# Performance work log

Measured on AMD Instinct MI355X. Metric: run time of the kernel, lower is better.

Reference implementation:

```python
import jax, jax.numpy as jnp
import numpy as np

# --- CSV_Architecture_v2 layout (mediapipe hands: 21 landmarks per hand) ---
INTRO = np.arange(0, 3)                 # vector_intro_idxs
H0_IDX, H0_PROB = 3, 4                  # handedness_0_idx, handedness_0_prob_idx
HAND0_X = np.arange(5, 26)
HAND0_Y = np.arange(26, 47)
HAND0_Z = np.arange(47, 68)
H1_IDX, H1_PROB = 68, 69
HAND1_X = np.arange(70, 91)
HAND1_Y = np.arange(91, 112)
HAND1_Z = np.arange(112, 133)
FRAME_REPR_LEN = 133
NO_HAND = -1.0                          # arch.no_hand_detected_val

B, S = 256, 2048


def setup_inputs() -> dict:
    key = jax.random.key(0)
    k1, k2, k3 = jax.random.split(key, 3)
    X = jax.random.normal(k1, (B, S, FRAME_REPR_LEN), dtype=jnp.float32)
    h0 = jnp.where(jax.random.bernoulli(k2, 0.3, (B, S)), NO_HAND, 1.0)
    h1 = jnp.where(jax.random.bernoulli(k3, 0.3, (B, S)), NO_HAND, 1.0)
    X = X.at[:, :, H0_IDX].set(h0).at[:, :, H1_IDX].set(h1)
    return {"X": X}


def _hand_sub_matrix(x, hidx, xi, yi, zi):
    """x: [S, F]. Build the per-hand subtraction matrix of strategy 'seq_on_last':
    find the MOST RECENT frame where this hand is valid, take its wrist (x,y,z),
    and subtract that wrist from this hand's coord columns on every valid frame."""
    S = x.shape[0]
    valid = x[:, hidx] != NO_HAND                      # [S] bool
    any_valid = jnp.any(valid)
    t = jnp.arange(S)
    last = jnp.maximum(jnp.max(jnp.where(valid, t, -1)), 0)  # last valid frame (safe)
    wrist_cols = jnp.array([xi[0], yi[0], zi[0]])
    ref = x[last, wrist_cols]                          # [3] reference wrist
    sub_vec = (jnp.zeros((x.shape[1],), x.dtype)
               .at[xi].set(ref[0])
               .at[yi].set(ref[1])
               .at[zi].set(ref[2]))                    # [F]
    row_mask = (valid & any_valid).astype(x.dtype)     # subtract only on valid frames
    return row_mask[:, None] * sub_vec[None, :]        # [S, F]


def reference(X):
    """Strategy 'seq_on_last': per sequence, per hand, normalize coords to the
    most recent valid wrist point. Vectorized over batch (original: tf.map_fn)."""
    def per_seq(x):  # x: [S, F]
        s0 = _hand_sub_matrix(x, H0_IDX, HAND0_X, HAND0_Y, HAND0_Z)
        s1 = _hand_sub_matrix(x, H1_IDX, HAND1_X, HAND1_Y, HAND1_Z)
        return x - (s0 + s1)
    return jax.vmap(per_seq)(X)
```

## Files before the change

kernel.cpp:

```cpp
#include <hip/hip_runtime.h>

#define SEQ 2048
#define FR  133
#define H0I 3
#define H1I 68
#define NOHAND -1.0f
#define BLK 1024

__global__ __launch_bounds__(BLK) void normalizer_kernel(
    const float* __restrict__ X, float* __restrict__ Out) {
    __shared__ unsigned char s_mask[SEQ];
    __shared__ float s_ref[6];
    __shared__ int s_red0[16], s_red1[16];

    const int b   = blockIdx.x;
    const int tid = threadIdx.x;
    const float* xb = X   + (size_t)b * (SEQ * FR);
    float*       ob = Out + (size_t)b * (SEQ * FR);

    int m0 = -1, m1 = -1;
    for (int t = tid; t < SEQ; t += BLK) {
        float v0 = xb[(size_t)t * FR + H0I];
        float v1 = xb[(size_t)t * FR + H1I];
        int b0 = (v0 != NOHAND);
        int b1 = (v1 != NOHAND);
        s_mask[t] = (unsigned char)(b0 | (b1 << 1));
        if (b0) m0 = t;
        if (b1) m1 = t;
    }
    #pragma unroll
    for (int off = 32; off > 0; off >>= 1) {
        m0 = max(m0, __shfl_down(m0, off, 64));
        m1 = max(m1, __shfl_down(m1, off, 64));
    }
    int wave = tid >> 6, lane = tid & 63;
    if (lane == 0) { s_red0[wave] = m0; s_red1[wave] = m1; }
    __syncthreads();
    if (tid == 0) {
        int a0 = -1, a1 = -1;
        #pragma unroll
        for (int w = 0; w < BLK / 64; ++w) {
            a0 = max(a0, s_red0[w]);
            a1 = max(a1, s_red1[w]);
        }
        int l0 = a0 < 0 ? 0 : a0;
        int l1 = a1 < 0 ? 0 : a1;
        s_ref[0] = xb[(size_t)l0 * FR + 5];
        s_ref[1] = xb[(size_t)l0 * FR + 26];
        s_ref[2] = xb[(size_t)l0 * FR + 47];
        s_ref[3] = xb[(size_t)l1 * FR + 70];
        s_ref[4] = xb[(size_t)l1 * FR + 91];
        s_ref[5] = xb[(size_t)l1 * FR + 112];
    }
    __syncthreads();
    const float r0x = s_ref[0], r0y = s_ref[1], r0z = s_ref[2];
    const float r1x = s_ref[3], r1y = s_ref[4], r1z = s_ref[5];

    const int NV = (SEQ * FR) / 4;
    const float4* xv = (const float4*)xb;
    float4*       ov = (float4*)ob;
    for (int i = tid; i < NV; i += BLK) {
        float4 v = xv[i];
        int e     = i * 4;
        int frame = (int)((unsigned)e / 133u);
        int f0    = e - frame * 133;
        float vals[4] = {v.x, v.y, v.z, v.w};
        #pragma unroll
        for (int j = 0; j < 4; ++j) {
            int f = f0 + j;
            int fr = frame;
            if (f >= FR) { f -= FR; fr += 1; }
            int mk = s_mask[fr];
            float sub = 0.f;
            if (f >= 5 && f < 68) {
                if (mk & 1) {
                    int k = (f >= 26) + (f >= 47);
                    sub = (k == 0) ? r0x : ((k == 1) ? r0y : r0z);
                }
            } else if (f >= 70) {
                if (mk & 2) {
                    int k = (f >= 91) + (f >= 112);
                    sub = (k == 0) ? r1x : ((k == 1) ? r1y : r1z);
                }
            }
            vals[j] -= sub;
        }
        float4 o; o.x = vals[0]; o.y = vals[1]; o.z = vals[2]; o.w = vals[3];
        ov[i] = o;
    }
}

extern "C" void kernel_launch(void* const* d_in, const int* in_sizes, int n_in,
                              void* d_out, int out_size, void* d_ws, size_t ws_size,
                              hipStream_t stream) {
    const float* X = (const float*)d_in[0];
    float* Out     = (float*)d_out;
    int nB = in_sizes[0] / (SEQ * FR);
    normalizer_kernel<<<nB, BLK, 0, stream>>>(X, Out);
}
```

Measured before the change: 125.0 us.

## Split into backward-scan refs kernel and chunked streaming kernel

Replaces the single per-sequence block with two kernels. The first uses one wave per sequence that scans backward with ballots and stops at the most recent valid frame for each hand, then writes the six wrist references to workspace. The second launches eight blocks per sequence, each handling a 256-frame chunk with its own local mask, which raises parallelism beyond the 256 blocks of the old launch. This adds a second launch and a workspace round trip, and the backward scan reads strided handedness values.

After: 127.6 us. 2.1% more time.

```diff
diff --git a/kernel.cpp b/kernel.cpp
--- a/kernel.cpp
+++ b/kernel.cpp
@@ -5,61 +5,70 @@
 #define H0I 3
 #define H1I 68
 #define NOHAND -1.0f
-#define BLK 1024
 
-__global__ __launch_bounds__(BLK) void normalizer_kernel(
-    const float* __restrict__ X, float* __restrict__ Out) {
-    __shared__ unsigned char s_mask[SEQ];
-    __shared__ float s_ref[6];
-    __shared__ int s_red0[16], s_red1[16];
+#define CH_FRAMES 256
+#define CH_ELEMS  (CH_FRAMES * FR)
+#define CH_VEC    (CH_ELEMS / 4)
+#define NCHUNK    (SEQ / CH_FRAMES)
 
-    const int b   = blockIdx.x;
-    const int tid = threadIdx.x;
-    const float* xb = X   + (size_t)b * (SEQ * FR);
-    float*       ob = Out + (size_t)b * (SEQ * FR);
+__global__ __launch_bounds__(64) void refs_kernel(
+    const float* __restrict__ X, float* __restrict__ refs ) {
+    const int b    = blockIdx.x;
+    const int lane = threadIdx.x;
+    const float* xb = X + (size_t)b * (SEQ * FR);
 
-    int m0 = -1, m1 = -1;
-    for (int t = tid; t < SEQ; t += BLK) {
+    int last0 = -1, last1 = -1;
+    for (int start = SEQ - 64; ; start -= 64) {
+        int t = start + lane;
         float v0 = xb[(size_t)t * FR + H0I];
         float v1 = xb[(size_t)t * FR + H1I];
-        int b0 = (v0 != NOHAND);
-        int b1 = (v1 != NOHAND);
-        s_mask[t] = (unsigned char)(b0 | (b1 << 1));
-        if (b0) m0 = t;
-        if (b1) m1 = t;
+        unsigned long long b0 = __ballot(v0 != NOHAND);
+        unsigned long long b1 = __ballot(v1 != NOHAND);
+        if (last0 < 0 && b0) last0 = start + 63 - __builtin_clzll(b0);
+        if (last1 < 0 && b1) last1 = start + 63 - __builtin_clzll(b1);
+        if ((last0 >= 0 && last1 >= 0) || start == 0) break;
     }
-    #pragma unroll
-    for (int off = 32; off > 0; off >>= 1) {
-        m0 = max(m0, __shfl_down(m0, off, 64));
-        m1 = max(m1, __shfl_down(m1, off, 64));
+    if (lane == 0) {
+        int l0 = last0 < 0 ? 0 : last0;
+        int l1 = last1 < 0 ? 0 : last1;
+        float* r = refs + b * 8;
+        r[0] = xb[(size_t)l0 * FR + 5];
+        r[1] = xb[(size_t)l0 * FR + 26];
+        r[2] = xb[(size_t)l0 * FR + 47];
+        r[3] = xb[(size_t)l1 * FR + 70];
+        r[4] = xb[(size_t)l1 * FR + 91];
+        r[5] = xb[(size_t)l1 * FR + 112];
     }
-    int wave = tid >> 6, lane = tid & 63;
-    if (lane == 0) { s_red0[wave] = m0; s_red1[wave] = m1; }
+}
+
+__global__ __launch_bounds__(256) void stream_kernel(
+    const float* __restrict__ X, float* __restrict__ Out,
+    const float* __restrict__ refs) {
+    __shared__ unsigned char s_mask[CH_FRAMES];
+    __shared__ float s_ref[6];
+
+    const int blk = blockIdx.x;
+    const int seq = blk >> 3;
+    const int ch  = blk & (NCHUNK - 1);
+    const int tid = threadIdx.x;
+
+    const float* xb = X   + (size_t)seq * (SEQ * FR) + (size_t)ch * CH_ELEMS;
+    float*       ob = Out + (size_t)seq * (SEQ * FR) + (size_t)ch * CH_ELEMS;
+
+    {
+        float v0 = xb[(size_t)tid * FR + H0I];
+        float v1 = xb[(size_t)tid * FR + H1I];
+        s_mask[tid] = (unsigned char)((v0 != NOHAND) | ((v1 != NOHAND) << 1));
+    }
+    if (tid < 6) s_ref[tid] = refs[seq * 8 + tid];
     __syncthreads();
-    if (tid == 0) {
-        int a0 = -1, a1 = -1;
-        #pragma unroll
-        for (int w = 0; w < BLK / 64; ++w) {
-            a0 = max(a0, s_red0[w]);
-            a1 = max(a1, s_red1[w]);
-        }
-        int l0 = a0 < 0 ? 0 : a0;
-        int l1 = a1 < 0 ? 0 : a1;
-        s_ref[0] = xb[(size_t)l0 * FR + 5];
-        s_ref[1] = xb[(size_t)l0 * FR + 26];
-        s_ref[2] = xb[(size_t)l0 * FR + 47];
-        s_ref[3] = xb[(size_t)l1 * FR + 70];
-        s_ref[4] = xb[(size_t)l1 * FR + 91];
-        s_ref[5] = xb[(size_t)l1 * FR + 112];
-    }
-    __syncthreads();
+
     const float r0x = s_ref[0], r0y = s_ref[1], r0z = s_ref[2];
     const float r1x = s_ref[3], r1y = s_ref[4], r1z = s_ref[5];
 
-    const int NV = (SEQ * FR) / 4;
     const float4* xv = (const float4*)xb;
     float4*       ov = (float4*)ob;
-    for (int i = tid; i < NV; i += BLK) {
+    for (int i = tid; i < CH_VEC; i += 256) {
         float4 v = xv[i];
         int e     = i * 4;
         int frame = (int)((unsigned)e / 133u);
@@ -95,6 +104,8 @@
                               hipStream_t stream) {
     const float* X = (const float*)d_in[0];
     float* Out     = (float*)d_out;
+    float* refs    = (float*)d_ws;
     int nB = in_sizes[0] / (SEQ * FR);
-    normalizer_kernel<<<nB, BLK, 0, stream>>>(X, Out);
+    refs_kernel<<<nB, 64, 0, stream>>>(X, refs);
+    stream_kernel<<<nB * NCHUNK, 256, 0, stream>>>(X, Out, refs);
 }
```
